# Optimization experiments

Measured on AMD Instinct MI355X. Metric: run time of the kernel, lower is better.

The kernel has to match this reference:

```python
import jax, jax.numpy as jnp
import numpy as np

OUT_SIZE, K0, K_MIN, K_MAX = 7, 4, 2, 5


def setup_inputs() -> dict:
    key = jax.random.key(0)
    ks = jax.random.split(key, 8)
    B, C, H, W, K = 4, 256, 800, 800, 512
    p2 = jax.random.normal(ks[0], (B, C, 200, 200), jnp.float32)
    p3 = jax.random.normal(ks[1], (B, C, 100, 100), jnp.float32)
    p4 = jax.random.normal(ks[2], (B, C, 50, 50), jnp.float32)
    p5 = jax.random.normal(ks[3], (B, C, 25, 25), jnp.float32)
    # boxes: centers uniform in image, sizes log-uniform in [16, 512] px
    cx = jax.random.uniform(ks[4], (B, K)) * W
    cy = jax.random.uniform(ks[5], (B, K)) * H
    logs = jax.random.uniform(ks[6], (B, K, 2), minval=np.log(16.0), maxval=np.log(512.0))
    wh = jnp.exp(logs)
    x1 = jnp.clip(cx - wh[..., 0] * 0.5, 0.0, W - 1.0)
    x2 = jnp.clip(cx + wh[..., 0] * 0.5, 0.0, float(W))
    y1 = jnp.clip(cy - wh[..., 1] * 0.5, 0.0, H - 1.0)
    y2 = jnp.clip(cy + wh[..., 1] * 0.5, 0.0, float(H))
    proposals = jnp.stack([x1, y1, jnp.maximum(x2, x1 + 1.0), jnp.maximum(y2, y1 + 1.0)], axis=-1)
    return {"p2": p2, "p3": p3, "p4": p4, "p5": p5, "proposals": proposals, "H": H, "W": W}


def _bilinear_border(fm_nhwc, b_idx, gx, gy):
    """grid_sample(mode=bilinear, align_corners=True, padding_mode=border).
    fm_nhwc: [B,Hf,Wf,C]; b_idx: [N]; gx,gy: [N,S,S] in [-1,1]. -> [N,S,S,C]"""
    Hf, Wf = fm_nhwc.shape[1], fm_nhwc.shape[2]
    x = jnp.clip((gx + 1.0) * 0.5 * (Wf - 1), 0.0, Wf - 1.0)
    y = jnp.clip((gy + 1.0) * 0.5 * (Hf - 1), 0.0, Hf - 1.0)
    x0 = jnp.floor(x)
    y0 = jnp.floor(y)
    wx = x - x0
    wy = y - y0
    xi0 = x0.astype(jnp.int32)
    yi0 = y0.astype(jnp.int32)
    xi1 = jnp.minimum(xi0 + 1, Wf - 1)
    yi1 = jnp.minimum(yi0 + 1, Hf - 1)
    b = b_idx[:, None, None]
    v00 = fm_nhwc[b, yi0, xi0]  # [N,S,S,C]
    v01 = fm_nhwc[b, yi0, xi1]
    v10 = fm_nhwc[b, yi1, xi0]
    v11 = fm_nhwc[b, yi1, xi1]
    wx = wx[..., None]
    wy = wy[..., None]
    top = v00 * (1.0 - wx) + v01 * wx
    bot = v10 * (1.0 - wx) + v11 * wx
    return top * (1.0 - wy) + bot * wy


def reference(p2, p3, p4, p5, proposals, H, W):
    B, K, _ = proposals.shape
    boxes = proposals.reshape(-1, 4)  # [N,4]
    N = boxes.shape[0]
    b_idx = jnp.repeat(jnp.arange(B, dtype=jnp.int32), K)
    # FPN level assignment: k = floor(k0 + log2(sqrt(area)/224)) clamped
    areas = jnp.sqrt(jnp.clip((boxes[:, 2] - boxes[:, 0]) * (boxes[:, 3] - boxes[:, 1]), 1e-6))
    lev = jnp.clip(jnp.floor(K0 + jnp.log2(areas / 224.0)), K_MIN, K_MAX).astype(jnp.int32) - K_MIN
    # normalized box corners in [-1,1]
    x1n = boxes[:, 0] / W * 2.0 - 1.0
    y1n = boxes[:, 1] / H * 2.0 - 1.0
    x2n = boxes[:, 2] / W * 2.0 - 1.0
    y2n = boxes[:, 3] / H * 2.0 - 1.0
    g = jnp.linspace(0.0, 1.0, OUT_SIZE)
    gy_g, gx_g = jnp.meshgrid(g, g, indexing="ij")  # [S,S]
    gx = x1n[:, None, None] + (x2n - x1n)[:, None, None] * gx_g[None]
    gy = y1n[:, None, None] + (y2n - y1n)[:, None, None] * gy_g[None]
    C = p2.shape[1]
    out = jnp.zeros((N, OUT_SIZE, OUT_SIZE, C), p2.dtype)
    for lvl, fm in enumerate([p2, p3, p4, p5]):
        crop = _bilinear_border(fm.transpose(0, 2, 3, 1), b_idx, gx, gy)
        out = out + jnp.where((lev == lvl)[:, None, None, None], crop, 0.0)
    return out.transpose(0, 3, 1, 2)  # [N,C,S,S]
```

## Files before the change

kernel.cpp:

```cpp
#include <hip/hip_runtime.h>

#define OUT_S 7
#define NPTS  49
#define C_CH  256
#define ELEMS (C_CH * NPTS)
#define ITERS (ELEMS / 256)
#define NXCD  8

__global__ __launch_bounds__(256, 8) void roi_align_fused(
    const float* __restrict__ p2, const float* __restrict__ p3,
    const float* __restrict__ p4, const float* __restrict__ p5,
    const float* __restrict__ prop, const int* __restrict__ Hp,
    const int* __restrict__ Wp, float* __restrict__ out, int K_per_img)
{
    __shared__ int4   s_off[NPTS];
    __shared__ float2 s_w[NPTS];

    const int nwg = gridDim.x;
    int n = blockIdx.x;
    if ((nwg & (NXCD - 1)) == 0) {
        const int q = nwg >> 3;
        n = (n & (NXCD - 1)) * q + (n >> 3);
    }

    const int t = threadIdx.x;
    const int b = n / K_per_img;

    const float W = (float)Wp[0];
    const float H = (float)Hp[0];

    const float4 box = reinterpret_cast<const float4*>(prop)[n];
    const float x1 = box.x, y1 = box.y, x2 = box.z, y2 = box.w;

    const float area = fmaxf((x2 - x1) * (y2 - y1), 1e-6f);
    const float sqa  = sqrtf(area);
    int lev = (int)floorf(4.0f + log2f(sqa / 224.0f));
    lev = min(max(lev, 2), 5);

    const float* fm; int Hf, Wf;
    if      (lev == 2) { fm = p2; Hf = 200; Wf = 200; }
    else if (lev == 3) { fm = p3; Hf = 100; Wf = 100; }
    else if (lev == 4) { fm = p4; Hf = 50;  Wf = 50;  }
    else               { fm = p5; Hf = 25;  Wf = 25;  }
    const int plane = Hf * Wf;

    if (t < NPTS) {
        const int iy = t / OUT_S;
        const int ix = t - iy * OUT_S;

        const float x1n = x1 / W * 2.0f - 1.0f;
        const float x2n = x2 / W * 2.0f - 1.0f;
        const float y1n = y1 / H * 2.0f - 1.0f;
        const float y2n = y2 / H * 2.0f - 1.0f;
        const float tx = (float)ix * (1.0f / 6.0f);
        const float ty = (float)iy * (1.0f / 6.0f);
        const float gx = x1n + (x2n - x1n) * tx;
        const float gy = y1n + (y2n - y1n) * ty;

        float x = (gx + 1.0f) * 0.5f * (float)(Wf - 1);
        float y = (gy + 1.0f) * 0.5f * (float)(Hf - 1);
        x = fminf(fmaxf(x, 0.0f), (float)(Wf - 1));
        y = fminf(fmaxf(y, 0.0f), (float)(Hf - 1));

        const float x0f = floorf(x), y0f = floorf(y);
        const float wx = x - x0f,  wy = y - y0f;
        const int xi0 = (int)x0f,  yi0 = (int)y0f;
        const int xi1 = min(xi0 + 1, Wf - 1);
        const int yi1 = min(yi0 + 1, Hf - 1);

        s_off[t] = make_int4(yi0 * Wf + xi0, yi0 * Wf + xi1,
                             yi1 * Wf + xi0, yi1 * Wf + xi1);
        s_w[t]   = make_float2(wx, wy);
    }
    __syncthreads();

    const float* basep = fm + (size_t)b * C_CH * (size_t)plane;
    float*       outp  = out + (size_t)n * ELEMS;

    #pragma unroll 4
    for (int j = 0; j < ITERS; ++j) {
        const int idx = t + 256 * j;
        const int c   = (unsigned)idx / NPTS;
        const int p   = idx - c * NPTS;

        const int4   o = s_off[p];
        const float2 w = s_w[p];

        const float* pb = basep + (size_t)c * plane;
        const float v00 = pb[o.x];
        const float v01 = pb[o.y];
        const float v10 = pb[o.z];
        const float v11 = pb[o.w];

        const float omwx = 1.0f - w.x, omwy = 1.0f - w.y;
        const float top = v00 * omwx + v01 * w.x;
        const float bot = v10 * omwx + v11 * w.x;
        const float r   = top * omwy + bot * w.y;

        __builtin_nontemporal_store(r, &outp[idx]);
    }
}

extern "C" void kernel_launch(void* const* d_in, const int* in_sizes, int n_in,
                              void* d_out, int out_size, void* d_ws, size_t ws_size,
                              hipStream_t stream) {
    const float* p2   = (const float*)d_in[0];
    const float* p3   = (const float*)d_in[1];
    const float* p4   = (const float*)d_in[2];
    const float* p5   = (const float*)d_in[3];
    const float* prop = (const float*)d_in[4];
    const int*   Hp   = (const int*)d_in[5];
    const int*   Wp   = (const int*)d_in[6];
    float* out = (float*)d_out;

    const int N = in_sizes[4] / 4;
    const int B = in_sizes[0] / (C_CH * 200 * 200);
    const int K = N / (B > 0 ? B : 1);

    roi_align_fused<<<N, 256, 0, stream>>>(p2, p3, p4, p5, prop, Hp, Wp, out, K);
}
```

Baseline: 404.1 us.

## Sort ROIs by (image, FPN level) before launching the crop kernel

Adds a single-block pre-kernel that buckets proposals by batch index and FPN level with a counting sort into workspace. The main kernel then maps block IDs to ROIs through this permutation, so blocks that run at the same time touch the same feature map and get more L2/MALL reuse. The cost is an extra serial kernel launch, an extra indirection load per block, and less balanced per-XCD work.

```diff
diff --git a/kernel.cpp b/kernel.cpp
--- a/kernel.cpp
+++ b/kernel.cpp
@@ -6,22 +6,66 @@
 #define ELEMS (C_CH * NPTS)
 #define ITERS (ELEMS / 256)
 #define NXCD  8
+#define MAXB  64
+
+__device__ __forceinline__ int roi_level(float x1, float y1, float x2, float y2) {
+    const float area = fmaxf((x2 - x1) * (y2 - y1), 1e-6f);
+    const float sqa  = sqrtf(area);
+    int lev = (int)floorf(4.0f + log2f(sqa / 224.0f));
+    return min(max(lev, 2), 5);
+}
+
+__global__ void build_order(const float* __restrict__ prop, int N, int K,
+                            int* __restrict__ order)
+{
+    __shared__ int s_cnt[MAXB];
+    __shared__ int s_off[MAXB];
+    const int t = threadIdx.x;
+    if (t < MAXB) s_cnt[t] = 0;
+    __syncthreads();
+
+    int myb[16];
+    const int per = (N + 255) / 256;
+    for (int i = 0; i < per; ++i) {
+        const int n = t + 256 * i;
+        if (n < N) {
+            const float4 bx = reinterpret_cast<const float4*>(prop)[n];
+            const int lev = roi_level(bx.x, bx.y, bx.z, bx.w);
+            const int b   = (n / K) * 4 + (lev - 2);
+            myb[i] = b;
+            atomicAdd(&s_cnt[b], 1);
+        }
+    }
+    __syncthreads();
+    if (t == 0) {
+        int acc = 0;
+        for (int j = 0; j < MAXB; ++j) { s_off[j] = acc; acc += s_cnt[j]; }
+    }
+    __syncthreads();
+    for (int i = 0; i < per; ++i) {
+        const int n = t + 256 * i;
+        if (n < N) {
+            const int pos = atomicAdd(&s_off[myb[i]], 1);
+            order[pos] = n;
+        }
+    }
+}
 
 __global__ __launch_bounds__(256, 8) void roi_align_fused(
     const float* __restrict__ p2, const float* __restrict__ p3,
     const float* __restrict__ p4, const float* __restrict__ p5,
     const float* __restrict__ prop, const int* __restrict__ Hp,
-    const int* __restrict__ Wp, float* __restrict__ out, int K_per_img)
+    const int* __restrict__ Wp, float* __restrict__ out, int K_per_img,
+    const int* __restrict__ order)
 {
-    __shared__ int4   s_off[NPTS];
+    __shared__ int4   s_offs[NPTS];
     __shared__ float2 s_w[NPTS];
 
     const int nwg = gridDim.x;
-    int n = blockIdx.x;
-    if ((nwg & (NXCD - 1)) == 0) {
-        const int q = nwg >> 3;
-        n = (n & (NXCD - 1)) * q + (n >> 3);
-    }
+    int m = blockIdx.x;
+    if ((nwg & (NXCD - 1)) == 0)
+        m = (m & (NXCD - 1)) * (nwg >> 3) + (m >> 3);
+    const int n = order ? order[m] : m;
 
     const int t = threadIdx.x;
     const int b = n / K_per_img;
@@ -32,10 +76,7 @@
     const float4 box = reinterpret_cast<const float4*>(prop)[n];
     const float x1 = box.x, y1 = box.y, x2 = box.z, y2 = box.w;
 
-    const float area = fmaxf((x2 - x1) * (y2 - y1), 1e-6f);
-    const float sqa  = sqrtf(area);
-    int lev = (int)floorf(4.0f + log2f(sqa / 224.0f));
-    lev = min(max(lev, 2), 5);
+    const int lev = roi_level(x1, y1, x2, y2);
 
     const float* fm; int Hf, Wf;
     if      (lev == 2) { fm = p2; Hf = 200; Wf = 200; }
@@ -68,9 +109,9 @@
         const int xi1 = min(xi0 + 1, Wf - 1);
         const int yi1 = min(yi0 + 1, Hf - 1);
 
-        s_off[t] = make_int4(yi0 * Wf + xi0, yi0 * Wf + xi1,
-                             yi1 * Wf + xi0, yi1 * Wf + xi1);
-        s_w[t]   = make_float2(wx, wy);
+        s_offs[t] = make_int4(yi0 * Wf + xi0, yi0 * Wf + xi1,
+                              yi1 * Wf + xi0, yi1 * Wf + xi1);
+        s_w[t]    = make_float2(wx, wy);
     }
     __syncthreads();
 
@@ -83,7 +124,7 @@
         const int c   = (unsigned)idx / NPTS;
         const int p   = idx - c * NPTS;
 
-        const int4   o = s_off[p];
+        const int4   o = s_offs[p];
         const float2 w = s_w[p];
 
         const float* pb = basep + (size_t)c * plane;
@@ -117,5 +158,11 @@
     const int B = in_sizes[0] / (C_CH * 200 * 200);
     const int K = N / (B > 0 ? B : 1);
 
-    roi_align_fused<<<N, 256, 0, stream>>>(p2, p3, p4, p5, prop, Hp, Wp, out, K);
+    int* order = nullptr;
+    if (ws_size >= (size_t)N * sizeof(int) && N <= 4096 && B * 4 <= MAXB) {
+        order = (int*)d_ws;
+        build_order<<<1, 256, 0, stream>>>(prop, N, K, order);
+    }
+    roi_align_fused<<<N, 256, 0, stream>>>(p2, p3, p4, p5, prop, Hp, Wp, out,
+                                           K, order);
 }
```

Measured after the change: 393.0 us. 1.03x faster.
